# Kernel optimization log

Measured on AMD Instinct MI355X. Metric: run time of the kernel, lower is better.

## Reference

```python
import jax, jax.numpy as jnp
import numpy as np

INPUT_SIZE = 512
HIDDEN_SIZE = 1024
BATCH = 16384


def setup_inputs() -> dict:
    key = jax.random.key(0)
    ks = jax.random.split(key, 11)
    s_x = 1.0 / np.sqrt(INPUT_SIZE)
    s_h = 1.0 / np.sqrt(HIDDEN_SIZE)
    inp = {
        "x": jax.random.normal(ks[0], (BATCH, INPUT_SIZE), dtype=jnp.float32),
        "hidden": jax.random.normal(ks[1], (BATCH, HIDDEN_SIZE), dtype=jnp.float32),
        # Linear weights stored as (in, out) for x @ W
        "Wxr": jax.random.uniform(ks[2], (INPUT_SIZE, HIDDEN_SIZE), jnp.float32, -s_x, s_x),
        "bxr": jax.random.uniform(ks[3], (HIDDEN_SIZE,), jnp.float32, -s_x, s_x),
        "Whr": jax.random.uniform(ks[4], (HIDDEN_SIZE, HIDDEN_SIZE), jnp.float32, -s_h, s_h),
        "Wxz": jax.random.uniform(ks[5], (INPUT_SIZE, HIDDEN_SIZE), jnp.float32, -s_x, s_x),
        "bxz": jax.random.uniform(ks[6], (HIDDEN_SIZE,), jnp.float32, -s_x, s_x),
        "Whz": jax.random.uniform(ks[7], (HIDDEN_SIZE, HIDDEN_SIZE), jnp.float32, -s_h, s_h),
        "Wxh": jax.random.uniform(ks[8], (INPUT_SIZE, HIDDEN_SIZE), jnp.float32, -s_x, s_x),
        "bxh": jax.random.uniform(ks[9], (HIDDEN_SIZE,), jnp.float32, -s_x, s_x),
        "Whh": jax.random.uniform(ks[10], (HIDDEN_SIZE, HIDDEN_SIZE), jnp.float32, -s_h, s_h),
    }
    return inp


def reference(x, hidden, Wxr, bxr, Whr, Wxz, bxz, Whz, Wxh, bxh, Whh):
    # GRU cell, single timestep.
    r = jax.nn.sigmoid(x @ Wxr + bxr + hidden @ Whr)          # reset gate (B,H)
    z = jax.nn.sigmoid(x @ Wxz + bxz + hidden @ Whz)          # update gate (B,H)
    h_cand = jnp.tanh(x @ Wxh + bxh + (r * hidden) @ Whh)     # candidate (B,H)
    return z * hidden + (1.0 - z) * h_cand
```

## Files before the change

### kernel.cpp

```cpp
#include <hip/hip_runtime.h>

typedef unsigned short u16;
typedef unsigned int u32;
typedef __bf16 bf16x8 __attribute__((ext_vector_type(8)));
typedef float f32x4 __attribute__((ext_vector_type(4)));

#define B_ROWS 16384
#define K1 1536

__device__ __forceinline__ u16 f2bf(float f) {
  u32 u = __float_as_uint(f);
  u = (u + 0x7fffu + ((u >> 16) & 1u)) >> 16;
  return (u16)u;
}
__device__ __forceinline__ float bf2f(u16 b) {
  return __uint_as_float(((u32)b) << 16);
}
__device__ __forceinline__ void gload_lds16(const void* g, void* l) {
  __builtin_amdgcn_global_load_lds((const __attribute__((address_space(1))) void*)g,
                                   (__attribute__((address_space(3))) void*)l,
                                   16, 0, 0);
}

__global__ void cvt_xh(const float* __restrict__ x, const float* __restrict__ h,
                       u16* __restrict__ xh) {
  const int iv = blockIdx.x * 256 + threadIdx.x;
  const int row = iv / 384;
  const int col = (iv - row * 384) * 4;
  const float* src = (col < 512) ? x + (size_t)row * 512 + col
                                 : h + (size_t)row * 1024 + (col - 512);
  float4 v = *(const float4*)src;
  u32 a = (u32)f2bf(v.x) | ((u32)f2bf(v.y) << 16);
  u32 b = (u32)f2bf(v.z) | ((u32)f2bf(v.w) << 16);
  *(uint2*)(xh + (size_t)row * 1536 + col) = make_uint2(a, b);
}

__global__ void transpose_cvt6(const float* __restrict__ Wxr, const float* __restrict__ Whr,
                               const float* __restrict__ Wxz, const float* __restrict__ Whz,
                               const float* __restrict__ Wxh, const float* __restrict__ Whh,
                               u16* __restrict__ W1t, u16* __restrict__ W2t) {
  __shared__ float tile[32][33];
  const int z = blockIdx.z;
  const float* W;
  u16* T;
  int Ks, koff, roff;
  switch (z) {
    case 0:  W = Wxr; T = W1t; Ks = 512;  koff = 0;   roff = 0;    break;
    case 1:  W = Whr; T = W1t; Ks = 1024; koff = 512; roff = 0;    break;
    case 2:  W = Wxz; T = W1t; Ks = 512;  koff = 0;   roff = 1024; break;
    case 3:  W = Whz; T = W1t; Ks = 1024; koff = 512; roff = 1024; break;
    case 4:  W = Wxh; T = W2t; Ks = 512;  koff = 0;   roff = 0;    break;
    default: W = Whh; T = W2t; Ks = 1024; koff = 512; roff = 0;    break;
  }
  const int bx = blockIdx.x, by = blockIdx.y;
  if (by * 32 >= Ks) return;
  const int tx = threadIdx.x, ty = threadIdx.y;
#pragma unroll
  for (int r = 0; r < 32; r += 8)
    tile[ty + r][tx] = W[(size_t)(by * 32 + ty + r) * 1024 + bx * 32 + tx];
  __syncthreads();
#pragma unroll
  for (int r = 0; r < 32; r += 8)
    T[(size_t)(roff + bx * 32 + ty + r) * K1 + koff + by * 32 + tx] = f2bf(tile[tx][ty + r]);
}

struct Src {
  const u16 *a0, *a1, *b0, *b1;
  int sa0, sa1, sb0, sb1, tsplit;
};

__device__ __forceinline__ const u16* gsrc(const u16* p0, const u16* p1, int s0, int s1,
                                           int tsplit, int t, int grow) {
  return (t < tsplit) ? p0 + (size_t)grow * s0 + t * 64
                      : p1 + (size_t)grow * s1 + (t - tsplit) * 64;
}

__device__ __forceinline__ void stage_half(const u16* p0, const u16* p1, int s0, int s1,
                                           int tsplit, int t, int rowbase, int h,
                                           char* matB, int c, int tid, int kswz) {
  char* lds = matB + c * 32768 + h * 16384 + ((tid >> 6) << 10);
  const int r = tid >> 3;
  const u16* g0 = gsrc(p0, p1, s0, s1, tsplit, t, rowbase + h * 128 + r) + kswz;
  const u16* g1 = gsrc(p0, p1, s0, s1, tsplit, t, rowbase + h * 128 + 64 + r) + kswz;
  gload_lds16(g0, lds);
  gload_lds16(g1, lds + 8192);
}

#define STAGE_A(t_, c_, h_) \
  stage_half(S.a0, S.a1, S.sa0, S.sa1, S.tsplit, (t_), brow, (h_), AsB, (c_), tid, kswz)
#define STAGE_B(t_, c_, h_) \
  stage_half(S.b0, S.b1, S.sb0, S.sb1, S.tsplit, (t_), bcol, (h_), BsB, (c_), tid, kswz)

__device__ __forceinline__ void gemm256(const Src& S, int nt, int brow, int bcol,
                                        u16* AsU, u16* BsU, f32x4 acc[8][4]) {
  const int tid = threadIdx.x;
  const int l = tid & 63;
  const int wid = tid >> 6;
  const int wr = wid >> 2, wc = wid & 3;
  const int lr = l & 15, kq = l >> 4;
  const int swzB = (lr & 7) * 16;
  const int kswz = ((tid & 7) ^ ((tid >> 3) & 7)) * 8;
  char* AsB = (char*)AsU;
  char* BsB = (char*)BsU;
  const int colK0 = (kq * 16) ^ swzB;
  const int colK1 = (64 + kq * 16) ^ swzB;
  int aRow[8], bRow[4];
#pragma unroll
  for (int m = 0; m < 8; ++m) aRow[m] = (wr * 128 + m * 16 + lr) * 128;
#pragma unroll
  for (int n = 0; n < 4; ++n) bRow[n] = (wc * 64 + n * 16 + lr) * 128;

  STAGE_A(0, 0, 0);
  STAGE_A(0, 0, 1);
  STAGE_B(0, 0, 0);
  STAGE_B(0, 0, 1);
  if (1 < nt) STAGE_A(1, 1, 0);
  asm volatile("s_waitcnt vmcnt(2)" ::: "memory");
  __builtin_amdgcn_s_barrier();
  asm volatile("" ::: "memory");

  for (int t = 0; t < nt; ++t) {
    const int c = t & 1;
    const int cb = c << 15;
    bf16x8 a[4][2], b[4][2];
    if (t + 1 < nt) {
      STAGE_A(t + 1, c ^ 1, 1);
      STAGE_B(t + 1, c ^ 1, 0);
      STAGE_B(t + 1, c ^ 1, 1);
    }
#pragma unroll
    for (int m = 0; m < 4; ++m) {
      a[m][0] = *(const bf16x8*)(AsB + cb + aRow[m] + colK0);
      a[m][1] = *(const bf16x8*)(AsB + cb + aRow[m] + colK1);
    }
#pragma unroll
    for (int n = 0; n < 2; ++n) {
      b[n][0] = *(const bf16x8*)(BsB + cb + bRow[n] + colK0);
      b[n][1] = *(const bf16x8*)(BsB + cb + bRow[n] + colK1);
    }
    __builtin_amdgcn_s_barrier();
    asm volatile("s_waitcnt lgkmcnt(0)" ::: "memory");
    __builtin_amdgcn_sched_barrier(0);
    __builtin_amdgcn_s_setprio(1);
#pragma unroll
    for (int kk = 0; kk < 2; ++kk)
#pragma unroll
      for (int m = 0; m < 4; ++m)
#pragma unroll
        for (int n = 0; n < 2; ++n)
          acc[m][n] = __builtin_amdgcn_mfma_f32_16x16x32_bf16(a[m][kk], b[n][kk], acc[m][n], 0, 0, 0);
    __builtin_amdgcn_s_setprio(0);
    __builtin_amdgcn_s_barrier();
    asm volatile("" ::: "memory");
#pragma unroll
    for (int n = 2; n < 4; ++n) {
      b[n][0] = *(const bf16x8*)(BsB + cb + bRow[n] + colK0);
      b[n][1] = *(const bf16x8*)(BsB + cb + bRow[n] + colK1);
    }
    __builtin_amdgcn_s_barrier();
    asm volatile("s_waitcnt lgkmcnt(0)" ::: "memory");
    __builtin_amdgcn_sched_barrier(0);
    __builtin_amdgcn_s_setprio(1);
#pragma unroll
    for (int kk = 0; kk < 2; ++kk)
#pragma unroll
      for (int m = 0; m < 4; ++m)
#pragma unroll
        for (int n = 2; n < 4; ++n)
          acc[m][n] = __builtin_amdgcn_mfma_f32_16x16x32_bf16(a[m][kk], b[n][kk], acc[m][n], 0, 0, 0);
    __builtin_amdgcn_s_setprio(0);
    __builtin_amdgcn_s_barrier();
    asm volatile("" ::: "memory");
#pragma unroll
    for (int m = 0; m < 4; ++m) {
      a[m][0] = *(const bf16x8*)(AsB + cb + aRow[m + 4] + colK0);
      a[m][1] = *(const bf16x8*)(AsB + cb + aRow[m + 4] + colK1);
    }
    __builtin_amdgcn_s_barrier();
    asm volatile("s_waitcnt lgkmcnt(0)" ::: "memory");
    __builtin_amdgcn_sched_barrier(0);
    __builtin_amdgcn_s_setprio(1);
#pragma unroll
    for (int kk = 0; kk < 2; ++kk)
#pragma unroll
      for (int m = 0; m < 4; ++m)
#pragma unroll
        for (int n = 2; n < 4; ++n)
          acc[m + 4][n] = __builtin_amdgcn_mfma_f32_16x16x32_bf16(a[m][kk], b[n][kk], acc[m + 4][n], 0, 0, 0);
    __builtin_amdgcn_s_setprio(0);
    __builtin_amdgcn_s_barrier();
    asm volatile("" ::: "memory");
    if (t + 2 < nt) STAGE_A(t + 2, c, 0);
    __builtin_amdgcn_s_setprio(1);
#pragma unroll
    for (int kk = 0; kk < 2; ++kk)
#pragma unroll
      for (int m = 0; m < 4; ++m)
#pragma unroll
        for (int n = 0; n < 2; ++n)
          acc[m + 4][n] = __builtin_amdgcn_mfma_f32_16x16x32_bf16(a[m][kk], b[n][kk], acc[m + 4][n], 0, 0, 0);
    __builtin_amdgcn_s_setprio(0);
    if (t + 2 < nt) { asm volatile("s_waitcnt vmcnt(2)" ::: "memory"); }
    else            { asm volatile("s_waitcnt vmcnt(0)" ::: "memory"); }
    __builtin_amdgcn_s_barrier();
    asm volatile("" ::: "memory");
  }
}

__global__ __launch_bounds__(512, 2) void gru_gemm1(
    const u16* __restrict__ xh, const u16* __restrict__ W1t,
    const float* __restrict__ bxr, const float* __restrict__ bxz,
    u16* __restrict__ rhb, u16* __restrict__ zb) {
  __shared__ __align__(16) u16 As[2 * 256 * 64];
  __shared__ __align__(16) u16 Bs[2 * 256 * 64];
  const int orig = blockIdx.x;
  const int wg = (orig & 7) * 64 + (orig >> 3);
  const int mt = wg & 63, jt = wg >> 6;
  const int brow = mt * 256;
  const int jcol = jt * 256;

  Src S;
  S.a0 = xh;  S.sa0 = K1; S.a1 = xh + 512;  S.sa1 = K1;
  S.b0 = W1t; S.sb0 = K1; S.b1 = W1t + 512; S.sb1 = K1;
  S.tsplit = 8;

  f32x4 acc[8][4] = {};
  gemm256(S, 24, brow, jcol, As, Bs, acc);

  const int l = threadIdx.x & 63;
  const int wid = threadIdx.x >> 6;
  const int wr = wid >> 2, wc = wid & 3;
  const int colb = jcol + wc * 64 + (l & 15);
  const int rowb = brow + wr * 128 + (l >> 4) * 4;
  if (jt < 4) {
#pragma unroll
    for (int n = 0; n < 4; ++n) {
      const int col = colb + n * 16;
      const float bias = bxr[col];
#pragma unroll
      for (int m = 0; m < 8; ++m)
#pragma unroll
        for (int j = 0; j < 4; ++j) {
          const int row = rowb + m * 16 + j;
          const float rg = 1.f / (1.f + __expf(-(acc[m][n][j] + bias)));
          const float hv = bf2f(xh[(size_t)row * K1 + 512 + col]);
          rhb[(size_t)row * 1024 + col] = f2bf(rg * hv);
        }
    }
  } else {
#pragma unroll
    for (int n = 0; n < 4; ++n) {
      const int col = colb + n * 16 - 1024;
      const float bias = bxz[col];
#pragma unroll
      for (int m = 0; m < 8; ++m)
#pragma unroll
        for (int j = 0; j < 4; ++j) {
          const int row = rowb + m * 16 + j;
          const float zg = 1.f / (1.f + __expf(-(acc[m][n][j] + bias)));
          zb[(size_t)row * 1024 + col] = f2bf(zg);
        }
    }
  }
}

__global__ __launch_bounds__(512, 2) void gru_gemm2(
    const u16* __restrict__ xh, const u16* __restrict__ rhb,
    const u16* __restrict__ W2t, const float* __restrict__ bxh,
    const u16* __restrict__ zb, const float* __restrict__ hidden,
    float* __restrict__ out) {
  __shared__ __align__(16) u16 As[2 * 256 * 64];
  __shared__ __align__(16) u16 Bs[2 * 256 * 64];
  const int orig = blockIdx.x;
  const int wg = (orig & 7) * 32 + (orig >> 3);
  const int mt = wg & 63, jt = wg >> 6;
  const int brow = mt * 256;
  const int jcol = jt * 256;

  Src S;
  S.a0 = xh;  S.sa0 = K1; S.a1 = rhb;       S.sa1 = 1024;
  S.b0 = W2t; S.sb0 = K1; S.b1 = W2t + 512; S.sb1 = K1;
  S.tsplit = 8;

  f32x4 acc[8][4] = {};
  gemm256(S, 24, brow, jcol, As, Bs, acc);

  const int l = threadIdx.x & 63;
  const int wid = threadIdx.x >> 6;
  const int wr = wid >> 2, wc = wid & 3;
  const int colb = jcol + wc * 64 + (l & 15);
  const int rowb = brow + wr * 128 + (l >> 4) * 4;
#pragma unroll
  for (int n = 0; n < 4; ++n) {
    const int col = colb + n * 16;
    const float bias = bxh[col];
#pragma unroll
    for (int m = 0; m < 8; ++m)
#pragma unroll
      for (int j = 0; j < 4; ++j) {
        const int row = rowb + m * 16 + j;
        const size_t idx = (size_t)row * 1024 + col;
        const float e = __expf(2.f * (acc[m][n][j] + bias));
        const float hc = 1.f - 2.f / (e + 1.f);
        const float z = bf2f(zb[idx]);
        const float h = hidden[idx];
        out[idx] = z * h + (1.f - z) * hc;
      }
  }
}

extern "C" void kernel_launch(void* const* d_in, const int* in_sizes, int n_in,
                              void* d_out, int out_size, void* d_ws, size_t ws_size,
                              hipStream_t stream) {
  const float* x      = (const float*)d_in[0];
  const float* hidden = (const float*)d_in[1];
  const float* Wxr = (const float*)d_in[2];
  const float* bxr = (const float*)d_in[3];
  const float* Whr = (const float*)d_in[4];
  const float* Wxz = (const float*)d_in[5];
  const float* bxz = (const float*)d_in[6];
  const float* Whz = (const float*)d_in[7];
  const float* Wxh = (const float*)d_in[8];
  const float* bxh = (const float*)d_in[9];
  const float* Whh = (const float*)d_in[10];
  float* out = (float*)d_out;
  (void)in_sizes; (void)n_in; (void)out_size; (void)ws_size;

  char* p = (char*)d_ws;
  u16* xh  = (u16*)p; p += (size_t)B_ROWS * K1 * 2;
  u16* W1t = (u16*)p; p += (size_t)2048 * K1 * 2;
  u16* W2t = (u16*)p; p += (size_t)1024 * K1 * 2;
  u16* rhb = (u16*)p; p += (size_t)B_ROWS * 1024 * 2;
  u16* zb  = (u16*)p; p += (size_t)B_ROWS * 1024 * 2;

  cvt_xh<<<B_ROWS * 384 / 256, 256, 0, stream>>>(x, hidden, xh);
  transpose_cvt6<<<dim3(32, 32, 6), dim3(32, 8), 0, stream>>>(
      Wxr, Whr, Wxz, Whz, Wxh, Whh, W1t, W2t);

  gru_gemm1<<<512, 512, 0, stream>>>(xh, W1t, bxr, bxz, rhb, zb);
  gru_gemm2<<<256, 512, 0, stream>>>(xh, rhb, W2t, bxh, zb, hidden, out);
}
```

Measured before the change: 298.4 us.

## Software-pipeline LDS fragment reads behind MFMA in GEMM main loop

Restructures the per-tile inner loop so that LDS reads of the next operand fragments are issued while MFMAs on already-loaded fragments run. The A(0-3)/B(0-1) fragments for the next tile are prefetched at the end of the current iteration. This removes several workgroup barriers per tile. It adds register pressure from holding separate a03/a47/b01/b23 fragment sets, which could hurt occupancy at launch_bounds(512,2).

```diff
diff --git a/kernel.cpp b/kernel.cpp
--- a/kernel.cpp
+++ b/kernel.cpp
@@ -91,6 +91,10 @@
 #define STAGE_B(t_, c_, h_) \
   stage_half(S.b0, S.b1, S.sb0, S.sb1, S.tsplit, (t_), bcol, (h_), BsB, (c_), tid, kswz)
 
+#define LGKM0_FENCE() do { \
+    asm volatile("s_waitcnt lgkmcnt(0)" ::: "memory"); \
+    __builtin_amdgcn_sched_barrier(0); } while (0)
+
 __device__ __forceinline__ void gemm256(const Src& S, int nt, int brow, int bcol,
                                         u16* AsU, u16* BsU, f32x4 acc[8][4]) {
   const int tid = threadIdx.x;
@@ -119,28 +123,48 @@
   __builtin_amdgcn_s_barrier();
   asm volatile("" ::: "memory");
 
+  bf16x8 a03[4][2], a47[4][2], b01[2][2], b23[2][2];
+#pragma unroll
+  for (int m = 0; m < 4; ++m) {
+    a03[m][0] = *(const bf16x8*)(AsB + aRow[m] + colK0);
+    a03[m][1] = *(const bf16x8*)(AsB + aRow[m] + colK1);
+  }
+#pragma unroll
+  for (int n = 0; n < 2; ++n) {
+    b01[n][0] = *(const bf16x8*)(BsB + bRow[n] + colK0);
+    b01[n][1] = *(const bf16x8*)(BsB + bRow[n] + colK1);
+  }
+  LGKM0_FENCE();
+
   for (int t = 0; t < nt; ++t) {
     const int c = t & 1;
     const int cb = c << 15;
-    bf16x8 a[4][2], b[4][2];
+    const int cb1 = (c ^ 1) << 15;
     if (t + 1 < nt) {
       STAGE_A(t + 1, c ^ 1, 1);
       STAGE_B(t + 1, c ^ 1, 0);
       STAGE_B(t + 1, c ^ 1, 1);
     }
 #pragma unroll
+    for (int n = 0; n < 2; ++n) {
+      b23[n][0] = *(const bf16x8*)(BsB + cb + bRow[n + 2] + colK0);
+      b23[n][1] = *(const bf16x8*)(BsB + cb + bRow[n + 2] + colK1);
+    }
+    __builtin_amdgcn_s_setprio(1);
+#pragma unroll
+    for (int kk = 0; kk < 2; ++kk)
+#pragma unroll
+      for (int m = 0; m < 4; ++m)
+#pragma unroll
+        for (int n = 0; n < 2; ++n)
+          acc[m][n] = __builtin_amdgcn_mfma_f32_16x16x32_bf16(a03[m][kk], b01[n][kk], acc[m][n], 0, 0, 0);
+    __builtin_amdgcn_s_setprio(0);
+    LGKM0_FENCE();
+#pragma unroll
     for (int m = 0; m < 4; ++m) {
-      a[m][0] = *(const bf16x8*)(AsB + cb + aRow[m] + colK0);
-      a[m][1] = *(const bf16x8*)(AsB + cb + aRow[m] + colK1);
-    }
-#pragma unroll
-    for (int n = 0; n < 2; ++n) {
-      b[n][0] = *(const bf16x8*)(BsB + cb + bRow[n] + colK0);
-      b[n][1] = *(const bf16x8*)(BsB + cb + bRow[n] + colK1);
-    }
-    __builtin_amdgcn_s_barrier();
-    asm volatile("s_waitcnt lgkmcnt(0)" ::: "memory");
-    __builtin_amdgcn_sched_barrier(0);
+      a47[m][0] = *(const bf16x8*)(AsB + cb + aRow[m + 4] + colK0);
+      a47[m][1] = *(const bf16x8*)(AsB + cb + aRow[m + 4] + colK1);
+    }
     __builtin_amdgcn_s_setprio(1);
 #pragma unroll
     for (int kk = 0; kk < 2; ++kk)
@@ -148,48 +172,10 @@
       for (int m = 0; m < 4; ++m)
 #pragma unroll
         for (int n = 0; n < 2; ++n)
-          acc[m][n] = __builtin_amdgcn_mfma_f32_16x16x32_bf16(a[m][kk], b[n][kk], acc[m][n], 0, 0, 0);
+          acc[m][n + 2] = __builtin_amdgcn_mfma_f32_16x16x32_bf16(a03[m][kk], b23[n][kk], acc[m][n + 2], 0, 0, 0);
     __builtin_amdgcn_s_setprio(0);
     __builtin_amdgcn_s_barrier();
-    asm volatile("" ::: "memory");
-#pragma unroll
-    for (int n = 2; n < 4; ++n) {
-      b[n][0] = *(const bf16x8*)(BsB + cb + bRow[n] + colK0);
-      b[n][1] = *(const bf16x8*)(BsB + cb + bRow[n] + colK1);
-    }
-    __builtin_amdgcn_s_barrier();
-    asm volatile("s_waitcnt lgkmcnt(0)" ::: "memory");
-    __builtin_amdgcn_sched_barrier(0);
-    __builtin_amdgcn_s_setprio(1);
-#pragma unroll
-    for (int kk = 0; kk < 2; ++kk)
-#pragma unroll
-      for (int m = 0; m < 4; ++m)
-#pragma unroll
-        for (int n = 2; n < 4; ++n)
-          acc[m][n] = __builtin_amdgcn_mfma_f32_16x16x32_bf16(a[m][kk], b[n][kk], acc[m][n], 0, 0, 0);
-    __builtin_amdgcn_s_setprio(0);
-    __builtin_amdgcn_s_barrier();
-    asm volatile("" ::: "memory");
-#pragma unroll
-    for (int m = 0; m < 4; ++m) {
-      a[m][0] = *(const bf16x8*)(AsB + cb + aRow[m + 4] + colK0);
-      a[m][1] = *(const bf16x8*)(AsB + cb + aRow[m + 4] + colK1);
-    }
-    __builtin_amdgcn_s_barrier();
-    asm volatile("s_waitcnt lgkmcnt(0)" ::: "memory");
-    __builtin_amdgcn_sched_barrier(0);
-    __builtin_amdgcn_s_setprio(1);
-#pragma unroll
-    for (int kk = 0; kk < 2; ++kk)
-#pragma unroll
-      for (int m = 0; m < 4; ++m)
-#pragma unroll
-        for (int n = 2; n < 4; ++n)
-          acc[m + 4][n] = __builtin_amdgcn_mfma_f32_16x16x32_bf16(a[m][kk], b[n][kk], acc[m + 4][n], 0, 0, 0);
-    __builtin_amdgcn_s_setprio(0);
-    __builtin_amdgcn_s_barrier();
-    asm volatile("" ::: "memory");
+    LGKM0_FENCE();
     if (t + 2 < nt) STAGE_A(t + 2, c, 0);
     __builtin_amdgcn_s_setprio(1);
 #pragma unroll
@@ -198,12 +184,34 @@
       for (int m = 0; m < 4; ++m)
 #pragma unroll
         for (int n = 0; n < 2; ++n)
-          acc[m + 4][n] = __builtin_amdgcn_mfma_f32_16x16x32_bf16(a[m][kk], b[n][kk], acc[m + 4][n], 0, 0, 0);
+          acc[m + 4][n + 2] = __builtin_amdgcn_mfma_f32_16x16x32_bf16(a47[m][kk], b23[n][kk], acc[m + 4][n + 2], 0, 0, 0);
+    __builtin_amdgcn_s_setprio(0);
+    __builtin_amdgcn_s_setprio(1);
+#pragma unroll
+    for (int kk = 0; kk < 2; ++kk)
+#pragma unroll
+      for (int m = 0; m < 4; ++m)
+#pragma unroll
+        for (int n = 0; n < 2; ++n)
+          acc[m + 4][n] = __builtin_amdgcn_mfma_f32_16x16x32_bf16(a47[m][kk], b01[n][kk], acc[m + 4][n], 0, 0, 0);
     __builtin_amdgcn_s_setprio(0);
     if (t + 2 < nt) { asm volatile("s_waitcnt vmcnt(2)" ::: "memory"); }
     else            { asm volatile("s_waitcnt vmcnt(0)" ::: "memory"); }
     __builtin_amdgcn_s_barrier();
     asm volatile("" ::: "memory");
+    if (t + 1 < nt) {
+#pragma unroll
+      for (int m = 0; m < 4; ++m) {
+        a03[m][0] = *(const bf16x8*)(AsB + cb1 + aRow[m] + colK0);
+        a03[m][1] = *(const bf16x8*)(AsB + cb1 + aRow[m] + colK1);
+      }
+#pragma unroll
+      for (int n = 0; n < 2; ++n) {
+        b01[n][0] = *(const bf16x8*)(BsB + cb1 + bRow[n] + colK0);
+        b01[n][1] = *(const bf16x8*)(BsB + cb1 + bRow[n] + colK1);
+      }
+      LGKM0_FENCE();
+    }
   }
 }
 
```

Measured after the change: 320.2 us. 1.07x slower.
